# Kernel tuning notes

Measured on AMD Instinct MI355X. Metric: run time of the kernel, lower is better.

Reference implementation:

```python
import jax, jax.numpy as jnp
import numpy as np

B, T, I, H, C = 8192, 784, 1, 30, 10


def setup_inputs() -> dict:
    key = jax.random.key(0)
    ks = jax.random.split(key, 7)
    s_ih = 1.0 / np.sqrt(H)
    return {
        "x": jax.random.normal(ks[0], (B, T, I), dtype=jnp.float32),
        "W_ih": jax.random.uniform(ks[1], (H, I), jnp.float32, -s_ih, s_ih),
        "W_hh": jax.random.uniform(ks[2], (H, H), jnp.float32, -s_ih, s_ih),
        "b_ih": jax.random.uniform(ks[3], (H,), jnp.float32, -s_ih, s_ih),
        "b_hh": jax.random.uniform(ks[4], (H,), jnp.float32, -s_ih, s_ih),
        "W_fc": jax.random.uniform(ks[5], (C, H), jnp.float32, -s_ih, s_ih),
        "b_fc": jax.random.uniform(ks[6], (C,), jnp.float32, -s_ih, s_ih),
    }


def reference(x, W_ih, W_hh, b_ih, b_hh, W_fc, b_fc):
    # x: [B, T, I] -> scan over time. h_t = tanh(x_t W_ih^T + b_ih + h W_hh^T + b_hh)
    xs = jnp.swapaxes(x, 0, 1)  # [T, B, I]
    h0 = jnp.zeros((x.shape[0], W_hh.shape[0]), dtype=x.dtype)
    bias = b_ih + b_hh  # [H]

    def step(h, xt):
        h_new = jnp.tanh(xt @ W_ih.T + h @ W_hh.T + bias)
        return h_new, None

    hT, _ = jax.lax.scan(step, h0, xs)  # hT: [B, H] == out[:, -1, :]
    return hT @ W_fc.T + b_fc  # [B, C]
```

## Files before the change

### kernel.cpp

```cpp
#include <hip/hip_runtime.h>


#define BB 8192
#define TT 784
#define HH 30
#define CC 10
#define NB 16
#define LSTR 36

typedef __attribute__((ext_vector_type(2))) float f32x2;

#define PK2(k0, k1)                                                          \
    asm volatile(                                                            \
        "v_mov_b32_dpp v40, %2 row_newbcast:" #k0 " row_mask:0xf bank_mask:0xf\n\t" \
        "v_mov_b32_dpp v41, %3 row_newbcast:" #k0 " row_mask:0xf bank_mask:0xf\n\t" \
        "v_mov_b32_dpp v42, %2 row_newbcast:" #k1 " row_mask:0xf bank_mask:0xf\n\t" \
        "v_mov_b32_dpp v43, %3 row_newbcast:" #k1 " row_mask:0xf bank_mask:0xf\n\t" \
        "v_pk_fma_f32 %0, %4, v[40:41], %0\n\t"                              \
        "v_pk_fma_f32 %1, %5, v[40:41], %1\n\t"                              \
        "v_pk_fma_f32 %0, %6, v[42:43], %0\n\t"                              \
        "v_pk_fma_f32 %1, %7, v[42:43], %1"                                  \
        : "+v"(acc0), "+v"(acc1)                                             \
        : "v"(h0), "v"(h1), "v"(w0p[k0]), "v"(w1p[k0]),                      \
          "v"(w0p[k1]), "v"(w1p[k1])                                         \
        : "v40", "v41", "v42", "v43")

#define PK1(k0)                                                              \
    asm volatile(                                                            \
        "v_mov_b32_dpp v40, %2 row_newbcast:" #k0 " row_mask:0xf bank_mask:0xf\n\t" \
        "v_mov_b32_dpp v41, %3 row_newbcast:" #k0 " row_mask:0xf bank_mask:0xf\n\t" \
        "s_nop 0\n\t"                                                        \
        "v_pk_fma_f32 %0, %4, v[40:41], %0\n\t"                              \
        "v_pk_fma_f32 %1, %5, v[40:41], %1"                                  \
        : "+v"(acc0), "+v"(acc1)                                             \
        : "v"(h0), "v"(h1), "v"(w0p[k0]), "v"(w1p[k0])                       \
        : "v40", "v41")

__global__ __launch_bounds__(256)
__attribute__((amdgpu_waves_per_eu(2, 2)))
void rnn_scan_kernel(const float* __restrict__ x,
                     const float* __restrict__ W_ih,
                     const float* __restrict__ W_hh,
                     const float* __restrict__ b_ih,
                     const float* __restrict__ b_hh,
                     const float* __restrict__ W_fc,
                     const float* __restrict__ b_fc,
                     float* __restrict__ out) {
    __shared__ float hbuf[NB * LSTR];

    const int tid = threadIdx.x;
    const int bl  = tid >> 4;
    const int r   = tid & 15;
    const int i0  = r * 2;
    const int b   = blockIdx.x * NB + bl;

    f32x2 w0p[15], w1p[15];
    const bool v0 = (i0 < HH), v1 = (i0 + 1 < HH);
#pragma unroll
    for (int k = 0; k < 15; ++k) {
        const int c0 = 2 * k, c1 = 2 * k + 1;
        w0p[k].x = v0 ? W_hh[i0 * HH + c0] : 0.0f;
        w0p[k].y = v0 ? W_hh[i0 * HH + c1] : 0.0f;
        w1p[k].x = v1 ? W_hh[(i0 + 1) * HH + c0] : 0.0f;
        w1p[k].y = v1 ? W_hh[(i0 + 1) * HH + c1] : 0.0f;
    }
    float bias0 = v0 ? (b_ih[i0] + b_hh[i0]) : 0.0f;
    float bias1 = v1 ? (b_ih[i0 + 1] + b_hh[i0 + 1]) : 0.0f;
    float wih0  = v0 ? W_ih[i0] : 0.0f;
    float wih1  = v1 ? W_ih[i0 + 1] : 0.0f;

#pragma unroll
    for (int k = 0; k < 15; ++k) {
        asm volatile("" : "+v"(w0p[k]));
        asm volatile("" : "+v"(w1p[k]));
    }
    asm volatile("" : "+v"(bias0));
    asm volatile("" : "+v"(bias1));
    asm volatile("" : "+v"(wih0));
    asm volatile("" : "+v"(wih1));

    float h0 = 0.0f, h1 = 0.0f;

    const float* xb = x + (size_t)b * TT;
    float4 xq = *(const float4*)(xb);

    for (int q = 0; q < TT / 4; ++q) {
        float4 nxt = (q + 1 < TT / 4) ? *(const float4*)(xb + (q + 1) * 4)
                                      : make_float4(0.f, 0.f, 0.f, 0.f);
#pragma unroll
        for (int u = 0; u < 4; ++u) {
            const float xt = (u == 0) ? xq.x : (u == 1) ? xq.y
                           : (u == 2) ? xq.z : xq.w;
            f32x2 acc0 = {fmaf(xt, wih0, bias0), 0.0f};
            f32x2 acc1 = {fmaf(xt, wih1, bias1), 0.0f};
            asm volatile("s_nop 1");
            PK2( 0,  1); PK2( 2,  3); PK2( 4,  5); PK2( 6,  7);
            PK2( 8,  9); PK2(10, 11); PK2(12, 13); PK1(14);
            const float acc0s = acc0.x + acc0.y;
            const float acc1s = acc1.x + acc1.y;
            h0 = 1.0f - 2.0f * __builtin_amdgcn_rcpf(__expf(2.0f * acc0s) + 1.0f);
            h1 = 1.0f - 2.0f * __builtin_amdgcn_rcpf(__expf(2.0f * acc1s) + 1.0f);
        }
        xq = nxt;
    }

    float* hp = &hbuf[bl * LSTR];
    *(float2*)&hp[i0] = make_float2(h0, h1);
    __builtin_amdgcn_wave_barrier();

    if (r < CC) {
        const int c = r;
        float acc = b_fc[c];
#pragma unroll
        for (int j = 0; j < HH; ++j)
            acc += W_fc[c * HH + j] * hp[j];
        out[(size_t)b * CC + c] = acc;
    }
}

extern "C" void kernel_launch(void* const* d_in, const int* in_sizes, int n_in,
                              void* d_out, int out_size, void* d_ws, size_t ws_size,
                              hipStream_t stream) {
    const float* x    = (const float*)d_in[0];
    const float* W_ih = (const float*)d_in[1];
    const float* W_hh = (const float*)d_in[2];
    const float* b_ih = (const float*)d_in[3];
    const float* b_hh = (const float*)d_in[4];
    const float* W_fc = (const float*)d_in[5];
    const float* b_fc = (const float*)d_in[6];

    hipLaunchKernelGGL(rnn_scan_kernel,
                       dim3(BB / NB), dim3(NB * 16), 0, stream,
                       x, W_ih, W_hh, b_ih, b_hh, W_fc, b_fc,
                       (float*)d_out);
}
```

Measured before the change: 339.7 us.

## Interleave two batch rows per lane to overlap tanh with matvec

Each 16-lane group now carries two independent batch sequences (A and B) and software-pipelines them. The tanh (exp plus rcp) of one sequence is scheduled between the DPP/pk_fma matvec chunks of the other, pinned in place with sched_barriers. This hides transcendental latency and the serial dependency chain within a single wave. In exchange the block is halved to 128 threads at one wave per EU, so there are fewer waves per SIMD to hide latency through occupancy. The final step of sequence B is completed after the loop.

```diff
diff --git a/kernel.cpp b/kernel.cpp
--- a/kernel.cpp
+++ b/kernel.cpp
@@ -5,39 +5,40 @@
 #define TT 784
 #define HH 30
 #define CC 10
-#define NB 16
+#define NBB 16
 #define LSTR 36
 
+#define SB() __builtin_amdgcn_sched_barrier(0)
+
 typedef __attribute__((ext_vector_type(2))) float f32x2;
 
-#define PK2(k0, k1)                                                          \
+#define PK2(H0, H1, A0, A1, K0, K1)                                          \
     asm volatile(                                                            \
-        "v_mov_b32_dpp v40, %2 row_newbcast:" #k0 " row_mask:0xf bank_mask:0xf\n\t" \
-        "v_mov_b32_dpp v41, %3 row_newbcast:" #k0 " row_mask:0xf bank_mask:0xf\n\t" \
-        "v_mov_b32_dpp v42, %2 row_newbcast:" #k1 " row_mask:0xf bank_mask:0xf\n\t" \
-        "v_mov_b32_dpp v43, %3 row_newbcast:" #k1 " row_mask:0xf bank_mask:0xf\n\t" \
+        "v_mov_b32_dpp v40, %2 row_newbcast:" #K0 " row_mask:0xf bank_mask:0xf\n\t" \
+        "v_mov_b32_dpp v41, %3 row_newbcast:" #K0 " row_mask:0xf bank_mask:0xf\n\t" \
+        "v_mov_b32_dpp v42, %2 row_newbcast:" #K1 " row_mask:0xf bank_mask:0xf\n\t" \
+        "v_mov_b32_dpp v43, %3 row_newbcast:" #K1 " row_mask:0xf bank_mask:0xf\n\t" \
         "v_pk_fma_f32 %0, %4, v[40:41], %0\n\t"                              \
         "v_pk_fma_f32 %1, %5, v[40:41], %1\n\t"                              \
         "v_pk_fma_f32 %0, %6, v[42:43], %0\n\t"                              \
         "v_pk_fma_f32 %1, %7, v[42:43], %1"                                  \
-        : "+v"(acc0), "+v"(acc1)                                             \
-        : "v"(h0), "v"(h1), "v"(w0p[k0]), "v"(w1p[k0]),                      \
-          "v"(w0p[k1]), "v"(w1p[k1])                                         \
+        : "+v"(A0), "+v"(A1)                                                 \
+        : "v"(H0), "v"(H1), "v"(w0p[K0]), "v"(w1p[K0]),                      \
+          "v"(w0p[K1]), "v"(w1p[K1])                                         \
         : "v40", "v41", "v42", "v43")
 
-#define PK1(k0)                                                              \
+#define PK1(H0, H1, A0, A1, K0)                                              \
     asm volatile(                                                            \
-        "v_mov_b32_dpp v40, %2 row_newbcast:" #k0 " row_mask:0xf bank_mask:0xf\n\t" \
-        "v_mov_b32_dpp v41, %3 row_newbcast:" #k0 " row_mask:0xf bank_mask:0xf\n\t" \
-        "s_nop 0\n\t"                                                        \
+        "v_mov_b32_dpp v40, %2 row_newbcast:" #K0 " row_mask:0xf bank_mask:0xf\n\t" \
+        "v_mov_b32_dpp v41, %3 row_newbcast:" #K0 " row_mask:0xf bank_mask:0xf\n\t" \
         "v_pk_fma_f32 %0, %4, v[40:41], %0\n\t"                              \
         "v_pk_fma_f32 %1, %5, v[40:41], %1"                                  \
-        : "+v"(acc0), "+v"(acc1)                                             \
-        : "v"(h0), "v"(h1), "v"(w0p[k0]), "v"(w1p[k0])                       \
+        : "+v"(A0), "+v"(A1)                                                 \
+        : "v"(H0), "v"(H1), "v"(w0p[K0]), "v"(w1p[K0])                       \
         : "v40", "v41")
 
-__global__ __launch_bounds__(256)
-__attribute__((amdgpu_waves_per_eu(2, 2)))
+__global__ __launch_bounds__(128)
+__attribute__((amdgpu_waves_per_eu(1, 1)))
 void rnn_scan_kernel(const float* __restrict__ x,
                      const float* __restrict__ W_ih,
                      const float* __restrict__ W_hh,
@@ -46,13 +47,17 @@
                      const float* __restrict__ W_fc,
                      const float* __restrict__ b_fc,
                      float* __restrict__ out) {
-    __shared__ float hbuf[NB * LSTR];
-
-    const int tid = threadIdx.x;
-    const int bl  = tid >> 4;
-    const int r   = tid & 15;
-    const int i0  = r * 2;
-    const int b   = blockIdx.x * NB + bl;
+    __shared__ float hbuf[NBB * LSTR];
+
+    const int tid  = threadIdx.x;
+    const int wv   = tid >> 6;
+    const int lane = tid & 63;
+    const int row  = lane >> 4;
+    const int r    = lane & 15;
+    const int i0   = r * 2;
+    const int lbA  = wv * 8 + row * 2;
+    const int bA   = blockIdx.x * NBB + lbA;
+    const int bB   = bA + 1;
 
     f32x2 w0p[15], w1p[15];
     const bool v0 = (i0 < HH), v1 = (i0 + 1 < HH);
@@ -79,42 +84,103 @@
     asm volatile("" : "+v"(wih0));
     asm volatile("" : "+v"(wih1));
 
-    float h0 = 0.0f, h1 = 0.0f;
-
-    const float* xb = x + (size_t)b * TT;
-    float4 xq = *(const float4*)(xb);
+    float hA0 = 0.0f, hA1 = 0.0f, hB0 = 0.0f, hB1 = 0.0f;
+    f32x2 accA0 = {0.f, 0.f}, accA1 = {0.f, 0.f};
+    f32x2 accB0 = {0.f, 0.f}, accB1 = {0.f, 0.f};
+
+    const float* xa = x + (size_t)bA * TT;
+    const float* xb = x + (size_t)bB * TT;
+    float4 xqA = *(const float4*)xa;
+    float4 xqB = *(const float4*)xb;
 
     for (int q = 0; q < TT / 4; ++q) {
-        float4 nxt = (q + 1 < TT / 4) ? *(const float4*)(xb + (q + 1) * 4)
-                                      : make_float4(0.f, 0.f, 0.f, 0.f);
+        const bool more = (q + 1 < TT / 4);
+        float4 nA = more ? *(const float4*)(xa + (q + 1) * 4) : make_float4(0,0,0,0);
+        float4 nB = more ? *(const float4*)(xb + (q + 1) * 4) : make_float4(0,0,0,0);
 #pragma unroll
         for (int u = 0; u < 4; ++u) {
-            const float xt = (u == 0) ? xq.x : (u == 1) ? xq.y
-                           : (u == 2) ? xq.z : xq.w;
-            f32x2 acc0 = {fmaf(xt, wih0, bias0), 0.0f};
-            f32x2 acc1 = {fmaf(xt, wih1, bias1), 0.0f};
-            asm volatile("s_nop 1");
-            PK2( 0,  1); PK2( 2,  3); PK2( 4,  5); PK2( 6,  7);
-            PK2( 8,  9); PK2(10, 11); PK2(12, 13); PK1(14);
-            const float acc0s = acc0.x + acc0.y;
-            const float acc1s = acc1.x + acc1.y;
-            h0 = 1.0f - 2.0f * __builtin_amdgcn_rcpf(__expf(2.0f * acc0s) + 1.0f);
-            h1 = 1.0f - 2.0f * __builtin_amdgcn_rcpf(__expf(2.0f * acc1s) + 1.0f);
+            const float xtA = (u == 0) ? xqA.x : (u == 1) ? xqA.y
+                            : (u == 2) ? xqA.z : xqA.w;
+            const float xtB = (u == 0) ? xqB.x : (u == 1) ? xqB.y
+                            : (u == 2) ? xqB.z : xqB.w;
+
+            accA0 = (f32x2){fmaf(xtA, wih0, bias0), 0.0f};
+            accA1 = (f32x2){fmaf(xtA, wih1, bias1), 0.0f};
+            SB();
+            PK2(hA0, hA1, accA0, accA1, 0, 1);
+            PK2(hA0, hA1, accA0, accA1, 2, 3);
+            PK2(hA0, hA1, accA0, accA1, 4, 5);
+            PK2(hA0, hA1, accA0, accA1, 6, 7);
+            const float sB0 = accB0.x + accB0.y;
+            const float sB1 = accB1.x + accB1.y;
+            SB();
+            PK2(hA0, hA1, accA0, accA1, 8, 9);
+            PK2(hA0, hA1, accA0, accA1, 10, 11);
+            const float eB0 = __expf(2.0f * sB0);
+            const float eB1 = __expf(2.0f * sB1);
+            SB();
+            PK2(hA0, hA1, accA0, accA1, 12, 13);
+            const float rB0 = __builtin_amdgcn_rcpf(eB0 + 1.0f);
+            const float rB1 = __builtin_amdgcn_rcpf(eB1 + 1.0f);
+            SB();
+            PK1(hA0, hA1, accA0, accA1, 14);
+            hB0 = 1.0f - 2.0f * rB0;
+            hB1 = 1.0f - 2.0f * rB1;
+            SB();
+
+            accB0 = (f32x2){fmaf(xtB, wih0, bias0), 0.0f};
+            accB1 = (f32x2){fmaf(xtB, wih1, bias1), 0.0f};
+            SB();
+            PK2(hB0, hB1, accB0, accB1, 0, 1);
+            PK2(hB0, hB1, accB0, accB1, 2, 3);
+            PK2(hB0, hB1, accB0, accB1, 4, 5);
+            PK2(hB0, hB1, accB0, accB1, 6, 7);
+            const float sA0 = accA0.x + accA0.y;
+            const float sA1 = accA1.x + accA1.y;
+            SB();
+            PK2(hB0, hB1, accB0, accB1, 8, 9);
+            PK2(hB0, hB1, accB0, accB1, 10, 11);
+            const float eA0 = __expf(2.0f * sA0);
+            const float eA1 = __expf(2.0f * sA1);
+            SB();
+            PK2(hB0, hB1, accB0, accB1, 12, 13);
+            const float rA0 = __builtin_amdgcn_rcpf(eA0 + 1.0f);
+            const float rA1 = __builtin_amdgcn_rcpf(eA1 + 1.0f);
+            SB();
+            PK1(hB0, hB1, accB0, accB1, 14);
+            hA0 = 1.0f - 2.0f * rA0;
+            hA1 = 1.0f - 2.0f * rA1;
+            SB();
         }
-        xq = nxt;
-    }
-
-    float* hp = &hbuf[bl * LSTR];
-    *(float2*)&hp[i0] = make_float2(h0, h1);
+        xqA = nA;
+        xqB = nB;
+    }
+
+    {
+        const float sB0 = accB0.x + accB0.y;
+        const float sB1 = accB1.x + accB1.y;
+        hB0 = 1.0f - 2.0f * __builtin_amdgcn_rcpf(__expf(2.0f * sB0) + 1.0f);
+        hB1 = 1.0f - 2.0f * __builtin_amdgcn_rcpf(__expf(2.0f * sB1) + 1.0f);
+    }
+
+    float* hpA = &hbuf[lbA * LSTR];
+    float* hpB = &hbuf[(lbA + 1) * LSTR];
+    *(float2*)&hpA[i0] = make_float2(hA0, hA1);
+    *(float2*)&hpB[i0] = make_float2(hB0, hB1);
     __builtin_amdgcn_wave_barrier();
 
     if (r < CC) {
         const int c = r;
-        float acc = b_fc[c];
-#pragma unroll
-        for (int j = 0; j < HH; ++j)
-            acc += W_fc[c * HH + j] * hp[j];
-        out[(size_t)b * CC + c] = acc;
+        float aA = b_fc[c];
+        float aB = b_fc[c];
+#pragma unroll
+        for (int j = 0; j < HH; ++j) {
+            const float wfc = W_fc[c * HH + j];
+            aA += wfc * hpA[j];
+            aB += wfc * hpB[j];
+        }
+        out[(size_t)bA * CC + c] = aA;
+        out[(size_t)bB * CC + c] = aB;
     }
 }
 
@@ -130,7 +196,7 @@
     const float* b_fc = (const float*)d_in[6];
 
     hipLaunchKernelGGL(rnn_scan_kernel,
-                       dim3(BB / NB), dim3(NB * 16), 0, stream,
+                       dim3(BB / NBB), dim3(128), 0, stream,
                        x, W_ih, W_hh, b_ih, b_hh, W_fc, b_fc,
                        (float*)d_out);
 }
```

New measurement: 347.5 us. 2.3% more time.
